# Kernel optimization log

Measured on AMD Instinct MI355X. Metric: run time of the kernel, lower is better.

Reference implementation:

```python
import jax, jax.numpy as jnp
import numpy as np

NUM_HEADS = 16
MASKED_BIAS = -10000.0


def setup_inputs() -> dict:
    key = jax.random.key(0)
    ks = jax.random.split(key, 5)
    B, S, D = 4, 2048, 1024
    return {
        "encodings": jax.random.normal(ks[0], (B, S, D), dtype=jnp.float32),
        "w_attn": jax.random.normal(ks[1], (D, 3 * D), dtype=jnp.float32) * (1.0 / np.sqrt(D)),
        "b_attn": jax.random.normal(ks[2], (3 * D,), dtype=jnp.float32) * 0.02,
        "w_proj": jax.random.normal(ks[3], (D, D), dtype=jnp.float32) * (1.0 / np.sqrt(D)),
        "b_proj": jax.random.normal(ks[4], (D,), dtype=jnp.float32) * 0.02,
    }


def reference(encodings, w_attn, b_attn, w_proj, b_proj):
    B, S, D = encodings.shape
    H = NUM_HEADS
    hs = D // H
    qkv = encodings @ w_attn + b_attn            # [B,S,3D]
    q, k, v = jnp.split(qkv, 3, axis=-1)
    # 'b s (h c) -> b h s c'
    def split_heads(x):
        return x.reshape(B, S, H, hs).transpose(0, 2, 1, 3)
    q, k, v = split_heads(q), split_heads(k), split_heads(v)
    # scores[b,h,f,t] = q[t] . k[f] / sqrt(hs)  (f=key, t=query)
    scores = jnp.einsum('bhtc,bhfc->bhft', q, k) / np.sqrt(hs).astype(jnp.float32)
    # causal: query t may attend key f iff t >= f  -> upper-tri in (f,t)
    causal = jnp.triu(jnp.ones((S, S), dtype=bool))  # [f,t]
    scores = jnp.where(causal[None, None], scores, jnp.asarray(MASKED_BIAS, scores.dtype))
    attn = jax.nn.softmax(scores, axis=-2)       # softmax over keys (f)
    ctx = jnp.einsum('bhft,bhfc->bhtc', attn, v)  # [B,H,S,hs]
    ctx = ctx.transpose(0, 2, 1, 3).reshape(B, S, D)  # 'b h s c -> b s (h c)'
    return ctx @ w_proj + b_proj
```

## Files before the change

kernel.cpp:

```cpp
#include <hip/hip_runtime.h>
#include <hip/hip_bf16.h>
#include <stdint.h>

#define NH  16
#define SEQ 2048
#define DM  1024
#define HS  64
#define NB  4

typedef __attribute__((ext_vector_type(8))) short bf16x8;
typedef __attribute__((ext_vector_type(4))) float f32x4;

__device__ __forceinline__ unsigned short f2b(float f) {
    unsigned int u = __float_as_uint(f);
    u += 0x7fffu + ((u >> 16) & 1u);
    return (unsigned short)(u >> 16);
}

__device__ __forceinline__ void gload16(const void* g, void* lds) {
    __builtin_amdgcn_global_load_lds(
        (const __attribute__((address_space(1))) unsigned int*)g,
        (__attribute__((address_space(3))) unsigned int*)lds,
        16, 0, 0);
}

__global__ void k_cvt(const float* __restrict__ in, unsigned short* __restrict__ out, int n) {
    int i = (blockIdx.x * blockDim.x + threadIdx.x) * 4;
    if (i >= n) return;
    float4 v = *(const float4*)(in + i);
    ushort4 o;
    o.x = f2b(v.x); o.y = f2b(v.y); o.z = f2b(v.z); o.w = f2b(v.w);
    *(ushort4*)(out + i) = o;
}

__global__ void k_tr(const float* __restrict__ in, unsigned short* __restrict__ out, int K, int N) {
    __shared__ float t[32][33];
    int n0 = blockIdx.x * 32, k0 = blockIdx.y * 32;
    int tx = threadIdx.x, ty = threadIdx.y;
#pragma unroll
    for (int j = 0; j < 32; j += 8)
        t[ty + j][tx] = in[(size_t)(k0 + ty + j) * N + n0 + tx];
    __syncthreads();
#pragma unroll
    for (int j = 0; j < 32; j += 8)
        out[(size_t)(n0 + ty + j) * K + k0 + tx] = f2b(t[tx][ty + j]);
}

template <int MODE>
__global__ __launch_bounds__(256, 2) void k_gemm(
    const unsigned short* __restrict__ A,
    const unsigned short* __restrict__ Bt,
    const float* __restrict__ bias,
    void* __restrict__ outp, int M, int N, int K)
{
    __shared__ unsigned short As[128 * 64];
    __shared__ unsigned short Bs[128 * 64];
    const int tid = threadIdx.x;
    const int l = tid & 63, w = tid >> 6;
    const int lg = l >> 4, li = l & 15;
    const int m0 = blockIdx.x * 128, n0 = blockIdx.y * 128;
    const int wm = (w >> 1) * 64, wn = (w & 1) * 64;

    f32x4 acc[4][4] = {};

    for (int k0 = 0; k0 < K; k0 += 64) {
#pragma unroll
        for (int i = 0; i < 4; i++) {
            int ch = i * 256 + tid;
            int row = ch >> 3, cc = ch & 7;
            int sc = cc ^ (row & 7);
            gload16(A + (size_t)(m0 + row) * K + k0 + sc * 8, &As[(i * 256 + w * 64) * 8]);
        }
#pragma unroll
        for (int i = 0; i < 4; i++) {
            int ch = i * 256 + tid;
            int row = ch >> 3, cc = ch & 7;
            int sc = cc ^ (row & 7);
            gload16(Bt + (size_t)(n0 + row) * K + k0 + sc * 8, &Bs[(i * 256 + w * 64) * 8]);
        }
        __syncthreads();
#pragma unroll
        for (int kc = 0; kc < 2; kc++) {
            bf16x8 af[4], bfr[4];
#pragma unroll
            for (int mi = 0; mi < 4; mi++) {
                int row = wm + mi * 16 + li;
                int chunk = (kc * 4 + lg) ^ (row & 7);
                af[mi] = *(const bf16x8*)&As[row * 64 + chunk * 8];
            }
#pragma unroll
            for (int ni = 0; ni < 4; ni++) {
                int row = wn + ni * 16 + li;
                int chunk = (kc * 4 + lg) ^ (row & 7);
                bfr[ni] = *(const bf16x8*)&Bs[row * 64 + chunk * 8];
            }
#pragma unroll
            for (int mi = 0; mi < 4; mi++)
#pragma unroll
                for (int ni = 0; ni < 4; ni++)
                    acc[mi][ni] = __builtin_amdgcn_mfma_f32_16x16x32_bf16(af[mi], bfr[ni], acc[mi][ni], 0, 0, 0);
        }
        __syncthreads();
    }

#pragma unroll
    for (int mi = 0; mi < 4; mi++) {
        int mrow = m0 + wm + mi * 16 + lg * 4;
#pragma unroll
        for (int ni = 0; ni < 4; ni++) {
            int col = n0 + wn + ni * 16 + li;
            float bv = bias[col];
            if (MODE == 0) {
                float* out = (float*)outp;
#pragma unroll
                for (int r = 0; r < 4; r++)
                    out[(size_t)(mrow + r) * N + col] = acc[mi][ni][r] + bv;
            } else {
                unsigned short* out = (unsigned short*)outp;
                int sqkv = col >> 10;
                int d = col & 1023;
                int h = d >> 6, c = d & 63;
                float scale = (sqkv == 0) ? 0.125f : 1.0f;
#pragma unroll
                for (int r = 0; r < 4; r++) {
                    int m = mrow + r;
                    int bq = m >> 11, sp = m & 2047;
                    size_t off = (size_t)sqkv * ((size_t)NB * NH * SEQ * HS) +
                                 ((size_t)(bq * NH + h) * SEQ + sp) * HS + c;
                    out[off] = f2b((acc[mi][ni][r] + bv) * scale);
                }
            }
        }
    }
}

__global__ __launch_bounds__(256, 2) void k_attn(
    const unsigned short* __restrict__ qkv,
    unsigned short* __restrict__ ctx)
{
    __shared__ unsigned short Ks[64 * 64];
    __shared__ unsigned short Vt[64 * 64];
    __shared__ unsigned short Ps[4 * 16 * 64];
    const int tid = threadIdx.x;
    const int l = tid & 63, w = tid >> 6;
    const int lg = l >> 4, li = l & 15;
    const int bh = blockIdx.x;
    const int q0 = blockIdx.y * 64;
    const size_t hb = (size_t)bh * SEQ * HS;
    const size_t QKV1 = (size_t)NB * NH * SEQ * HS;
    const unsigned short* Qg = qkv + hb;
    const unsigned short* Kg = qkv + QKV1 + hb;
    const unsigned short* Vg = qkv + 2 * QKV1 + hb;

    bf16x8 aq[2];
    {
        int t = q0 + w * 16 + li;
        aq[0] = *(const bf16x8*)(Qg + (size_t)t * HS + lg * 8);
        aq[1] = *(const bf16x8*)(Qg + (size_t)t * HS + 32 + lg * 8);
    }

    f32x4 acc[4] = {};
    float mr[4] = {-1e30f, -1e30f, -1e30f, -1e30f};
    float ls[4] = {0.f, 0.f, 0.f, 0.f};
    const int ntiles = q0 / 64 + 1;

    for (int ft = 0; ft < ntiles; ft++) {
        int f0 = ft * 64;
#pragma unroll
        for (int i = 0; i < 2; i++) {
            int ch = i * 256 + tid;
            int row = ch >> 3, cc = ch & 7;
            int sc = cc ^ (row & 7);
            gload16(Kg + (size_t)(f0 + row) * HS + sc * 8, &Ks[(i * 256 + w * 64) * 8]);
        }
#pragma unroll
        for (int i = 0; i < 2; i++) {
            int ch = i * 256 + tid;
            int fl = ch >> 3, c0 = (ch & 7) * 8;
            bf16x8 v = *(const bf16x8*)(Vg + (size_t)(f0 + fl) * HS + c0);
#pragma unroll
            for (int j = 0; j < 8; j++) {
                int c = c0 + j;
                int off = (c * 128 + fl * 2) ^ ((c & 7) << 4);
                *(unsigned short*)((char*)Vt + off) = ((unsigned short*)&v)[j];
            }
        }
        __syncthreads();

        f32x4 sa[4] = {};
#pragma unroll
        for (int kc = 0; kc < 2; kc++)
#pragma unroll
            for (int nt = 0; nt < 4; nt++) {
                int row = nt * 16 + li;
                int chunk = (kc * 4 + lg) ^ (row & 7);
                bf16x8 bk = *(const bf16x8*)&Ks[row * 64 + chunk * 8];
                sa[nt] = __builtin_amdgcn_mfma_f32_16x16x32_bf16(aq[kc], bk, sa[nt], 0, 0, 0);
            }

        if (ft == ntiles - 1) {
            int tb = q0 + w * 16 + lg * 4;
#pragma unroll
            for (int nt = 0; nt < 4; nt++) {
                int f = f0 + nt * 16 + li;
#pragma unroll
                for (int r = 0; r < 4; r++)
                    if (f > tb + r) sa[nt][r] = -1e30f;
            }
        }

        float corr[4];
#pragma unroll
        for (int r = 0; r < 4; r++) {
            float rm = fmaxf(fmaxf(sa[0][r], sa[1][r]), fmaxf(sa[2][r], sa[3][r]));
            rm = fmaxf(rm, __shfl_xor(rm, 1));
            rm = fmaxf(rm, __shfl_xor(rm, 2));
            rm = fmaxf(rm, __shfl_xor(rm, 4));
            rm = fmaxf(rm, __shfl_xor(rm, 8));
            float mn = fmaxf(mr[r], rm);
            corr[r] = __expf(mr[r] - mn);
            mr[r] = mn;
        }
        float rs[4] = {0.f, 0.f, 0.f, 0.f};
#pragma unroll
        for (int nt = 0; nt < 4; nt++)
#pragma unroll
            for (int r = 0; r < 4; r++) {
                float p = __expf(sa[nt][r] - mr[r]);
                sa[nt][r] = p;
                rs[r] += p;
            }
#pragma unroll
        for (int r = 0; r < 4; r++) {
            rs[r] += __shfl_xor(rs[r], 1);
            rs[r] += __shfl_xor(rs[r], 2);
            rs[r] += __shfl_xor(rs[r], 4);
            rs[r] += __shfl_xor(rs[r], 8);
            ls[r] = ls[r] * corr[r] + rs[r];
        }
#pragma unroll
        for (int nt = 0; nt < 4; nt++)
#pragma unroll
            for (int r = 0; r < 4; r++)
                acc[nt][r] *= corr[r];

#pragma unroll
        for (int nt = 0; nt < 4; nt++)
#pragma unroll
            for (int r = 0; r < 4; r++) {
                int row = lg * 4 + r, fl = nt * 16 + li;
                int off = (row * 128 + fl * 2) ^ ((row & 7) << 4);
                *(unsigned short*)((char*)Ps + w * 2048 + off) = f2b(sa[nt][r]);
            }
        __syncthreads();

#pragma unroll
        for (int kc = 0; kc < 2; kc++) {
            int pchunk = (kc * 4 + lg) ^ (li & 7);
            bf16x8 pf = *(const bf16x8*)((char*)Ps + w * 2048 + li * 128 + pchunk * 16);
#pragma unroll
            for (int nt = 0; nt < 4; nt++) {
                int c = nt * 16 + li;
                int vchunk = (kc * 4 + lg) ^ (c & 7);
                bf16x8 vf = *(const bf16x8*)((char*)Vt + c * 128 + vchunk * 16);
                acc[nt] = __builtin_amdgcn_mfma_f32_16x16x32_bf16(pf, vf, acc[nt], 0, 0, 0);
            }
        }
        __syncthreads();
    }

    int b = bh >> 4, h = bh & 15;
#pragma unroll
    for (int nt = 0; nt < 4; nt++)
#pragma unroll
        for (int r = 0; r < 4; r++) {
            int t = q0 + w * 16 + lg * 4 + r;
            int c = nt * 16 + li;
            float v = acc[nt][r] / ls[r];
            ctx[((size_t)(b * SEQ + t)) * DM + h * HS + c] = f2b(v);
        }
}

extern "C" void kernel_launch(void* const* d_in, const int* in_sizes, int n_in,
                              void* d_out, int out_size, void* d_ws, size_t ws_size,
                              hipStream_t stream) {
    const float* enc    = (const float*)d_in[0];
    const float* w_attn = (const float*)d_in[1];
    const float* b_attn = (const float*)d_in[2];
    const float* w_proj = (const float*)d_in[3];
    const float* b_proj = (const float*)d_in[4];
    float* out = (float*)d_out;

    unsigned short* ws = (unsigned short*)d_ws;
    unsigned short* X    = ws;
    unsigned short* Wq   = ws + 8388608;
    unsigned short* Wp   = Wq + 3145728;
    unsigned short* QKV  = Wp + 1048576;
    unsigned short* CTX  = X;

    const int M = NB * SEQ;

    k_cvt<<<8192, 256, 0, stream>>>(enc, X, M * DM);
    k_tr<<<dim3(96, 32), dim3(32, 8), 0, stream>>>(w_attn, Wq, DM, 3 * DM);
    k_tr<<<dim3(32, 32), dim3(32, 8), 0, stream>>>(w_proj, Wp, DM, DM);
    k_gemm<1><<<dim3(M / 128, 24), 256, 0, stream>>>(X, Wq, b_attn, QKV, M, 3 * DM, DM);
    k_attn<<<dim3(NB * NH, SEQ / 64), 256, 0, stream>>>(QKV, CTX);
    k_gemm<0><<<dim3(M / 128, 8), 256, 0, stream>>>(CTX, Wp, b_proj, out, M, DM, DM);
}
```

Measured before the change: 354.4 us.

## Store V transposed from QKV GEMM and process two query tiles per attention block

The QKV GEMM epilogue now writes V in a transposed [c][seq] layout, so the attention kernel can load it straight into LDS with async global-to-LDS copies instead of scattering a per-thread transpose. Each attention block now handles 128 queries as two 64-row tiles that share every loaded K/V tile, halving K/V traffic per query. Blocks are scheduled heaviest-first by reversing the query index, which should help causal load balance. It also drops one barrier per tile and relaxes the launch bounds, at the cost of more registers, possibly lower occupancy, and strided scalar writes for V in the GEMM epilogue.

```diff
diff --git a/kernel.cpp b/kernel.cpp
--- a/kernel.cpp
+++ b/kernel.cpp
@@ -117,6 +117,7 @@
                     out[(size_t)(mrow + r) * N + col] = acc[mi][ni][r] + bv;
             } else {
                 unsigned short* out = (unsigned short*)outp;
+                const size_t QKV1 = (size_t)NB * NH * SEQ * HS;
                 int sqkv = col >> 10;
                 int d = col & 1023;
                 int h = d >> 6, c = d & 63;
@@ -125,8 +126,11 @@
                 for (int r = 0; r < 4; r++) {
                     int m = mrow + r;
                     int bq = m >> 11, sp = m & 2047;
-                    size_t off = (size_t)sqkv * ((size_t)NB * NH * SEQ * HS) +
-                                 ((size_t)(bq * NH + h) * SEQ + sp) * HS + c;
+                    size_t off;
+                    if (sqkv == 2)
+                        off = 2 * QKV1 + ((size_t)(bq * NH + h) * HS + c) * SEQ + sp;
+                    else
+                        off = (size_t)sqkv * QKV1 + ((size_t)(bq * NH + h) * SEQ + sp) * HS + c;
                     out[off] = f2b((acc[mi][ni][r] + bv) * scale);
                 }
             }
@@ -134,35 +138,40 @@
     }
 }
 
-__global__ __launch_bounds__(256, 2) void k_attn(
+__global__ __launch_bounds__(256) void k_attn(
     const unsigned short* __restrict__ qkv,
     unsigned short* __restrict__ ctx)
 {
     __shared__ unsigned short Ks[64 * 64];
-    __shared__ unsigned short Vt[64 * 64];
-    __shared__ unsigned short Ps[4 * 16 * 64];
+    __shared__ unsigned short Vts[64 * 64];
+    __shared__ unsigned short Ps[4 * 32 * 64];
     const int tid = threadIdx.x;
     const int l = tid & 63, w = tid >> 6;
     const int lg = l >> 4, li = l & 15;
     const int bh = blockIdx.x;
-    const int q0 = blockIdx.y * 64;
+    const int q0 = (gridDim.y - 1 - blockIdx.y) * 128;
     const size_t hb = (size_t)bh * SEQ * HS;
     const size_t QKV1 = (size_t)NB * NH * SEQ * HS;
     const unsigned short* Qg = qkv + hb;
     const unsigned short* Kg = qkv + QKV1 + hb;
-    const unsigned short* Vg = qkv + 2 * QKV1 + hb;
-
-    bf16x8 aq[2];
-    {
-        int t = q0 + w * 16 + li;
-        aq[0] = *(const bf16x8*)(Qg + (size_t)t * HS + lg * 8);
-        aq[1] = *(const bf16x8*)(Qg + (size_t)t * HS + 32 + lg * 8);
+    const unsigned short* VTg = qkv + 2 * QKV1 + hb;
+
+    bf16x8 aq[2][2];
+#pragma unroll
+    for (int rt = 0; rt < 2; rt++) {
+        int t = q0 + rt * 64 + w * 16 + li;
+        aq[rt][0] = *(const bf16x8*)(Qg + (size_t)t * HS + lg * 8);
+        aq[rt][1] = *(const bf16x8*)(Qg + (size_t)t * HS + 32 + lg * 8);
     }
 
-    f32x4 acc[4] = {};
-    float mr[4] = {-1e30f, -1e30f, -1e30f, -1e30f};
-    float ls[4] = {0.f, 0.f, 0.f, 0.f};
-    const int ntiles = q0 / 64 + 1;
+    f32x4 acc[2][4] = {};
+    float mr[2][4], ls[2][4];
+#pragma unroll
+    for (int rt = 0; rt < 2; rt++)
+#pragma unroll
+        for (int r = 0; r < 4; r++) { mr[rt][r] = -1e30f; ls[rt][r] = 0.f; }
+
+    const int ntiles = q0 / 64 + 2;
 
     for (int ft = 0; ft < ntiles; ft++) {
         int f0 = ft * 64;
@@ -176,94 +185,94 @@
 #pragma unroll
         for (int i = 0; i < 2; i++) {
             int ch = i * 256 + tid;
-            int fl = ch >> 3, c0 = (ch & 7) * 8;
-            bf16x8 v = *(const bf16x8*)(Vg + (size_t)(f0 + fl) * HS + c0);
-#pragma unroll
-            for (int j = 0; j < 8; j++) {
-                int c = c0 + j;
-                int off = (c * 128 + fl * 2) ^ ((c & 7) << 4);
-                *(unsigned short*)((char*)Vt + off) = ((unsigned short*)&v)[j];
-            }
+            int row = ch >> 3, cc = ch & 7;
+            int sc = cc ^ (row & 7);
+            gload16(VTg + (size_t)row * SEQ + f0 + sc * 8, &Vts[(i * 256 + w * 64) * 8]);
         }
         __syncthreads();
 
-        f32x4 sa[4] = {};
-#pragma unroll
-        for (int kc = 0; kc < 2; kc++)
-#pragma unroll
-            for (int nt = 0; nt < 4; nt++) {
-                int row = nt * 16 + li;
-                int chunk = (kc * 4 + lg) ^ (row & 7);
-                bf16x8 bk = *(const bf16x8*)&Ks[row * 64 + chunk * 8];
-                sa[nt] = __builtin_amdgcn_mfma_f32_16x16x32_bf16(aq[kc], bk, sa[nt], 0, 0, 0);
-            }
-
-        if (ft == ntiles - 1) {
-            int tb = q0 + w * 16 + lg * 4;
-#pragma unroll
-            for (int nt = 0; nt < 4; nt++) {
-                int f = f0 + nt * 16 + li;
+#pragma unroll
+        for (int rt = 0; rt < 2; rt++) {
+            const int tb = q0 + rt * 64 + w * 16;
+            if (f0 > tb + 15) continue;
+
+            f32x4 sa[4] = {};
+#pragma unroll
+            for (int kc = 0; kc < 2; kc++)
+#pragma unroll
+                for (int nt = 0; nt < 4; nt++) {
+                    int row = nt * 16 + li;
+                    int chunk = (kc * 4 + lg) ^ (row & 7);
+                    bf16x8 bk = *(const bf16x8*)&Ks[row * 64 + chunk * 8];
+                    sa[nt] = __builtin_amdgcn_mfma_f32_16x16x32_bf16(aq[rt][kc], bk, sa[nt], 0, 0, 0);
+                }
+
+            if (f0 + 63 > tb) {
+                int trow = tb + lg * 4;
+#pragma unroll
+                for (int nt = 0; nt < 4; nt++) {
+                    int f = f0 + nt * 16 + li;
+#pragma unroll
+                    for (int r = 0; r < 4; r++)
+                        if (f > trow + r) sa[nt][r] = -1e30f;
+                }
+            }
+
+            float corr[4];
+#pragma unroll
+            for (int r = 0; r < 4; r++) {
+                float rm = fmaxf(fmaxf(sa[0][r], sa[1][r]), fmaxf(sa[2][r], sa[3][r]));
+                rm = fmaxf(rm, __shfl_xor(rm, 1));
+                rm = fmaxf(rm, __shfl_xor(rm, 2));
+                rm = fmaxf(rm, __shfl_xor(rm, 4));
+                rm = fmaxf(rm, __shfl_xor(rm, 8));
+                float mn = fmaxf(mr[rt][r], rm);
+                corr[r] = __expf(mr[rt][r] - mn);
+                mr[rt][r] = mn;
+            }
+            float rs[4] = {0.f, 0.f, 0.f, 0.f};
+#pragma unroll
+            for (int nt = 0; nt < 4; nt++)
+#pragma unroll
+                for (int r = 0; r < 4; r++) {
+                    float p = __expf(sa[nt][r] - mr[rt][r]);
+                    sa[nt][r] = p;
+                    rs[r] += p;
+                }
+#pragma unroll
+            for (int r = 0; r < 4; r++) {
+                rs[r] += __shfl_xor(rs[r], 1);
+                rs[r] += __shfl_xor(rs[r], 2);
+                rs[r] += __shfl_xor(rs[r], 4);
+                rs[r] += __shfl_xor(rs[r], 8);
+                ls[rt][r] = ls[rt][r] * corr[r] + rs[r];
+            }
+#pragma unroll
+            for (int nt = 0; nt < 4; nt++)
 #pragma unroll
                 for (int r = 0; r < 4; r++)
-                    if (f > tb + r) sa[nt][r] = -1e30f;
-            }
-        }
-
-        float corr[4];
-#pragma unroll
-        for (int r = 0; r < 4; r++) {
-            float rm = fmaxf(fmaxf(sa[0][r], sa[1][r]), fmaxf(sa[2][r], sa[3][r]));
-            rm = fmaxf(rm, __shfl_xor(rm, 1));
-            rm = fmaxf(rm, __shfl_xor(rm, 2));
-            rm = fmaxf(rm, __shfl_xor(rm, 4));
-            rm = fmaxf(rm, __shfl_xor(rm, 8));
-            float mn = fmaxf(mr[r], rm);
-            corr[r] = __expf(mr[r] - mn);
-            mr[r] = mn;
-        }
-        float rs[4] = {0.f, 0.f, 0.f, 0.f};
-#pragma unroll
-        for (int nt = 0; nt < 4; nt++)
-#pragma unroll
-            for (int r = 0; r < 4; r++) {
-                float p = __expf(sa[nt][r] - mr[r]);
-                sa[nt][r] = p;
-                rs[r] += p;
-            }
-#pragma unroll
-        for (int r = 0; r < 4; r++) {
-            rs[r] += __shfl_xor(rs[r], 1);
-            rs[r] += __shfl_xor(rs[r], 2);
-            rs[r] += __shfl_xor(rs[r], 4);
-            rs[r] += __shfl_xor(rs[r], 8);
-            ls[r] = ls[r] * corr[r] + rs[r];
-        }
-#pragma unroll
-        for (int nt = 0; nt < 4; nt++)
-#pragma unroll
-            for (int r = 0; r < 4; r++)
-                acc[nt][r] *= corr[r];
-
-#pragma unroll
-        for (int nt = 0; nt < 4; nt++)
-#pragma unroll
-            for (int r = 0; r < 4; r++) {
-                int row = lg * 4 + r, fl = nt * 16 + li;
-                int off = (row * 128 + fl * 2) ^ ((row & 7) << 4);
-                *(unsigned short*)((char*)Ps + w * 2048 + off) = f2b(sa[nt][r]);
-            }
-        __syncthreads();
-
-#pragma unroll
-        for (int kc = 0; kc < 2; kc++) {
-            int pchunk = (kc * 4 + lg) ^ (li & 7);
-            bf16x8 pf = *(const bf16x8*)((char*)Ps + w * 2048 + li * 128 + pchunk * 16);
-#pragma unroll
-            for (int nt = 0; nt < 4; nt++) {
-                int c = nt * 16 + li;
-                int vchunk = (kc * 4 + lg) ^ (c & 7);
-                bf16x8 vf = *(const bf16x8*)((char*)Vt + c * 128 + vchunk * 16);
-                acc[nt] = __builtin_amdgcn_mfma_f32_16x16x32_bf16(pf, vf, acc[nt], 0, 0, 0);
+                    acc[rt][nt][r] *= corr[r];
+
+            char* PB = (char*)Ps + w * 4096 + rt * 2048;
+#pragma unroll
+            for (int nt = 0; nt < 4; nt++)
+#pragma unroll
+                for (int r = 0; r < 4; r++) {
+                    int row = lg * 4 + r, f = nt * 16 + li;
+                    *(unsigned short*)(PB + row * 128 + ((f * 2) ^ ((row & 7) << 4))) = f2b(sa[nt][r]);
+                }
+
+#pragma unroll
+            for (int kc = 0; kc < 2; kc++) {
+                int C = kc * 4 + lg;
+                bf16x8 pf = *(const bf16x8*)(PB + li * 128 + ((C * 16) ^ ((li & 7) << 4)));
+#pragma unroll
+                for (int nt = 0; nt < 4; nt++) {
+                    int c = nt * 16 + li;
+                    int vch = C ^ (c & 7);
+                    bf16x8 vf = *(const bf16x8*)&Vts[c * 64 + vch * 8];
+                    acc[rt][nt] = __builtin_amdgcn_mfma_f32_16x16x32_bf16(pf, vf, acc[rt][nt], 0, 0, 0);
+                }
             }
         }
         __syncthreads();
@@ -271,14 +280,16 @@
 
     int b = bh >> 4, h = bh & 15;
 #pragma unroll
-    for (int nt = 0; nt < 4; nt++)
-#pragma unroll
-        for (int r = 0; r < 4; r++) {
-            int t = q0 + w * 16 + lg * 4 + r;
-            int c = nt * 16 + li;
-            float v = acc[nt][r] / ls[r];
-            ctx[((size_t)(b * SEQ + t)) * DM + h * HS + c] = f2b(v);
-        }
+    for (int rt = 0; rt < 2; rt++)
+#pragma unroll
+        for (int nt = 0; nt < 4; nt++)
+#pragma unroll
+            for (int r = 0; r < 4; r++) {
+                int t = q0 + rt * 64 + w * 16 + lg * 4 + r;
+                int c = nt * 16 + li;
+                float v = acc[rt][nt][r] / ls[rt][r];
+                ctx[((size_t)(b * SEQ + t)) * DM + h * HS + c] = f2b(v);
+            }
 }
 
 extern "C" void kernel_launch(void* const* d_in, const int* in_sizes, int n_in,
@@ -304,6 +315,6 @@
     k_tr<<<dim3(96, 32), dim3(32, 8), 0, stream>>>(w_attn, Wq, DM, 3 * DM);
     k_tr<<<dim3(32, 32), dim3(32, 8), 0, stream>>>(w_proj, Wp, DM, DM);
     k_gemm<1><<<dim3(M / 128, 24), 256, 0, stream>>>(X, Wq, b_attn, QKV, M, 3 * DM, DM);
-    k_attn<<<dim3(NB * NH, SEQ / 64), 256, 0, stream>>>(QKV, CTX);
+    k_attn<<<dim3(NB * NH, SEQ / 64 / 2), 256, 0, stream>>>(QKV, CTX);
     k_gemm<0><<<dim3(M / 128, 8), 256, 0, stream>>>(CTX, Wp, b_proj, out, M, DM, DM);
 }
```

After: 322.3 us. 9.1% less time.
